# Optimization experiments

Measured on AMD Instinct MI355X. Metric: run time of the kernel, lower is better.

## Reference

```python
import jax, jax.numpy as jnp
import numpy as np

B, M, E, K = 2048, 768, 16384, 32
EPS = 1e-8  # torch F.cosine_similarity default eps


def setup_inputs() -> dict:
    key = jax.random.key(0)
    ks = jax.random.split(key, 13)
    s_m = 1.0 / np.sqrt(M)  # nn.Linear(M, E) init bound
    s_e = 1.0 / np.sqrt(E)  # nn.Linear(E, M) init bound
    u = lambda k, shape, s: jax.random.uniform(k, shape, jnp.float32, -s, s)
    return {
        "x": jax.random.normal(ks[0], (B, M), jnp.float32),
        "enc_w": u(ks[1], (E, M), s_m), "enc_b": u(ks[2], (E,), s_m),
        "dec_w": u(ks[3], (M, E), s_e), "dec_b": u(ks[4], (M,), s_e),
        "enc1_w": u(ks[5], (E, M), s_m), "enc1_b": u(ks[6], (E,), s_m),
        "dec1_w": u(ks[7], (M, E), s_e), "dec1_b": u(ks[8], (M,), s_e),
        "enc2_w": u(ks[9], (E, M), s_m), "enc2_b": u(ks[10], (E,), s_m),
        "dec2_w": u(ks[11], (M, E), s_e), "dec2_b": u(ks[12], (M,), s_e),
        "k": K,
    }


def _aux_loss(a_BE, win_BE, c1_BE, c2_BE, dp_ME, d1_ME, d2_ME):
    # Faithful reduction of the B x M x E cosine-similarity along M:
    #   scaled_parent[b,:,e] = dp[:,e]*a[b,e];  scaled_child uses d1/d2 per winner mask.
    # cos_sim needs only M-dim dot products / norms of decoder columns.
    np2_E = jnp.sum(dp_ME * dp_ME, axis=0)   # ||dp_e||^2
    n1_E = jnp.sum(d1_ME * d1_ME, axis=0)
    n2_E = jnp.sum(d2_ME * d2_ME, axis=0)
    dp1_E = jnp.sum(dp_ME * d1_ME, axis=0)   # <dp_e, d1_e>
    dp2_E = jnp.sum(dp_ME * d2_ME, axis=0)
    c_BE = jnp.where(win_BE, c1_BE, c2_BE)
    dpc_BE = jnp.where(win_BE, dp1_E, dp2_E)
    nc_BE = jnp.where(win_BE, n1_E, n2_E)
    a2 = a_BE * a_BE
    dot = a2 * np2_E + a_BE * c_BE * dpc_BE                      # <parent, parent+child>
    norm_p = jnp.abs(a_BE) * jnp.sqrt(np2_E)                     # ||parent||
    comb2 = a2 * np2_E + 2.0 * a_BE * c_BE * dpc_BE + c_BE * c_BE * nc_BE
    norm_c = jnp.sqrt(jnp.maximum(comb2, 0.0))                   # ||parent+child||
    cos = dot / (jnp.maximum(norm_p, EPS) * jnp.maximum(norm_c, EPS))
    active = a_BE > 0
    return -jnp.sum(jnp.where(active, cos, 0.0)) / a_BE.shape[0]


def reference(x, enc_w, enc_b, dec_w, dec_b, enc1_w, enc1_b, dec1_w, dec1_b,
              enc2_w, enc2_b, dec2_w, dec2_b, k):
    Bn = x.shape[0]
    En = enc_w.shape[0]
    pre_BE = x @ enc_w.T + enc_b
    vals, idx = jax.lax.top_k(pre_BE, k)                         # [B,k]
    sae_BE = jnp.zeros_like(pre_BE).at[jnp.arange(Bn)[:, None], idx].set(vals)
    num_live_parent = jnp.zeros((En,), bool).at[idx.ravel()].set(True).sum()

    pre1_BE = x @ enc1_w.T + enc1_b
    pre2_BE = x @ enc2_w.T + enc2_b
    active = sae_BE != 0.0
    m1_BE = jnp.where(active, pre1_BE, 0.0)
    m2_BE = jnp.where(active, pre2_BE, 0.0)
    win_BE = m1_BE > m2_BE
    f1_BE = jnp.where(win_BE, m1_BE, 0.0)
    f2_BE = jnp.where(~win_BE, m2_BE, 0.0)
    num_live_c1 = jnp.any(f1_BE != 0, axis=0).sum()
    num_live_c2 = jnp.any(f2_BE != 0, axis=0).sum()

    recon_BM = (sae_BE @ dec_w.T + dec_b) + (f1_BE @ dec1_w.T + dec1_b) + (f2_BE @ dec2_w.T + dec2_b)

    sg = jax.lax.stop_gradient
    aux = _aux_loss(sg(sae_BE), sg(win_BE), sg(f1_BE), sg(f2_BE), dec_w, dec1_w, dec2_w)
    return recon_BM, (num_live_parent, num_live_c1, num_live_c2), aux
```

## Files before the change

kernel.cpp:

```cpp
#include <hip/hip_runtime.h>
#include <cstdint>
#include <cstddef>

#define B_N 2048
#define M_N 768
#define E_N 16384
#define K_N 32
#define EPSF 1e-8f

typedef __attribute__((ext_vector_type(8))) short short8;
typedef __attribute__((ext_vector_type(4))) float floatx4;
typedef __attribute__((ext_vector_type(4))) unsigned short ushort4v;

__device__ inline unsigned short f2bf(float f) {
  unsigned int u = __float_as_uint(f);
  unsigned int r = (u + 0x7fffu + ((u >> 16) & 1u)) >> 16;
  return (unsigned short)r;
}
__device__ inline float bf2f(unsigned short h) {
  return __uint_as_float(((unsigned int)h) << 16);
}

__global__ __launch_bounds__(256) void split2_kernel(
    const float* __restrict__ inA, unsigned short* __restrict__ hiA,
    unsigned short* __restrict__ loA, int n4A,
    const float* __restrict__ inB, unsigned short* __restrict__ hiB,
    unsigned short* __restrict__ loB, int n4B) {
  int i = blockIdx.x * 256 + threadIdx.x;
  const float* in;
  unsigned short* hi;
  unsigned short* lo;
  int idx;
  if (i < n4A) {
    in = inA; hi = hiA; lo = loA; idx = i;
  } else {
    idx = i - n4A;
    if (idx >= n4B) return;
    in = inB; hi = hiB; lo = loB;
  }
  float4 v = ((const float4*)in)[idx];
  ushort4v h, l;
  h.x = f2bf(v.x); l.x = f2bf(v.x - bf2f(h.x));
  h.y = f2bf(v.y); l.y = f2bf(v.y - bf2f(h.y));
  h.z = f2bf(v.z); l.z = f2bf(v.z - bf2f(h.z));
  h.w = f2bf(v.w); l.w = f2bf(v.w - bf2f(h.w));
  ((ushort4v*)hi)[idx] = h;
  ((ushort4v*)lo)[idx] = l;
}

__global__ __launch_bounds__(256) void prep_dec_kernel(
    const float* __restrict__ dw, const float* __restrict__ d1,
    const float* __restrict__ d2,
    float* __restrict__ dT0, float* __restrict__ dT1,
    float* __restrict__ dT2, float* __restrict__ stats) {
  __shared__ float t0[32][36], t1[32][36], t2[32][36];
  int tid = threadIdx.x;
  int e0 = blockIdx.x * 32;
  int m0 = blockIdx.y * 32;

  {
    int ml = tid >> 3, e4 = tid & 7;
    size_t gbase = (size_t)(m0 + ml) * E_N + e0 + e4 * 4;
    float4 a  = *(const float4*)&dw[gbase];
    float4 b1 = *(const float4*)&d1[gbase];
    float4 b2 = *(const float4*)&d2[gbase];
    *(float4*)&t0[ml][e4 * 4] = a;
    *(float4*)&t1[ml][e4 * 4] = b1;
    *(float4*)&t2[ml][e4 * 4] = b2;
  }
  __syncthreads();

  int el = tid >> 3, m4 = tid & 7;
  float4 v0, v1, v2;
  float s0 = 0.f, s1 = 0.f, s2 = 0.f, s3 = 0.f, s4 = 0.f;
#pragma unroll
  for (int j = 0; j < 4; ++j) {
    float A  = t0[m4 * 4 + j][el];
    float B1 = t1[m4 * 4 + j][el];
    float B2 = t2[m4 * 4 + j][el];
    ((float*)&v0)[j] = A;
    ((float*)&v1)[j] = B1;
    ((float*)&v2)[j] = B2;
    s0 = fmaf(A, A, s0);
    s1 = fmaf(B1, B1, s1);
    s2 = fmaf(B2, B2, s2);
    s3 = fmaf(A, B1, s3);
    s4 = fmaf(A, B2, s4);
  }
  size_t tbase = (size_t)(e0 + el) * M_N + m0 + m4 * 4;
  *(float4*)&dT0[tbase] = v0;
  *(float4*)&dT1[tbase] = v1;
  *(float4*)&dT2[tbase] = v2;

#pragma unroll
  for (int off = 1; off < 8; off <<= 1) {
    s0 += __shfl_xor(s0, off);
    s1 += __shfl_xor(s1, off);
    s2 += __shfl_xor(s2, off);
    s3 += __shfl_xor(s3, off);
    s4 += __shfl_xor(s4, off);
  }
  if (m4 == 0) {
    int e = e0 + el;
    atomicAdd(&stats[e], s0);
    atomicAdd(&stats[E_N + e], s1);
    atomicAdd(&stats[2 * E_N + e], s2);
    atomicAdd(&stats[3 * E_N + e], s3);
    atomicAdd(&stats[4 * E_N + e], s4);
  }
}

#define TM 128
#define TN 128
#define TK 32
#define LDK 40

__global__ __launch_bounds__(256) void gemm_mfma_kernel(
    const unsigned short* __restrict__ Ahi, const unsigned short* __restrict__ Alo,
    const unsigned short* __restrict__ Bhi, const unsigned short* __restrict__ Blo,
    const float* __restrict__ bias, float* __restrict__ C) {
  __shared__ __align__(16) unsigned short As_hi[TM * LDK];
  __shared__ __align__(16) unsigned short As_lo[TM * LDK];
  __shared__ __align__(16) unsigned short Bs_hi[TM * LDK];
  __shared__ __align__(16) unsigned short Bs_lo[TM * LDK];

  int tid = threadIdx.x;
  int lane = tid & 63;
  int wave = tid >> 6;
  int i0 = blockIdx.y * TM;
  int j0 = blockIdx.x * TN;
  int wm = (wave >> 1) * 64;
  int wn = (wave & 1) * 64;

  int row0 = tid >> 2, c40 = tid & 3;
  int row1 = 64 + (tid >> 2), c41 = tid & 3;
  const unsigned short* pAhi0 = Ahi + (size_t)(i0 + row0) * M_N + c40 * 8;
  const unsigned short* pAhi1 = Ahi + (size_t)(i0 + row1) * M_N + c41 * 8;
  const unsigned short* pAlo0 = Alo + (size_t)(i0 + row0) * M_N + c40 * 8;
  const unsigned short* pAlo1 = Alo + (size_t)(i0 + row1) * M_N + c41 * 8;
  const unsigned short* pBhi0 = Bhi + (size_t)(j0 + row0) * M_N + c40 * 8;
  const unsigned short* pBhi1 = Bhi + (size_t)(j0 + row1) * M_N + c41 * 8;
  const unsigned short* pBlo0 = Blo + (size_t)(j0 + row0) * M_N + c40 * 8;
  const unsigned short* pBlo1 = Blo + (size_t)(j0 + row1) * M_N + c41 * 8;
  int l0 = row0 * LDK + c40 * 8;
  int l1 = row1 * LDK + c41 * 8;

  floatx4 acc[4][4];
#pragma unroll
  for (int i = 0; i < 4; ++i)
#pragma unroll
    for (int j = 0; j < 4; ++j) acc[i][j] = (floatx4){0.f, 0.f, 0.f, 0.f};

  int fr = lane & 15;
  int fk = (lane >> 4) * 8;

  short8 vAh0 = *(const short8*)pAhi0;
  short8 vAh1 = *(const short8*)pAhi1;
  short8 vAl0 = *(const short8*)pAlo0;
  short8 vAl1 = *(const short8*)pAlo1;
  short8 vBh0 = *(const short8*)pBhi0;
  short8 vBh1 = *(const short8*)pBhi1;
  short8 vBl0 = *(const short8*)pBlo0;
  short8 vBl1 = *(const short8*)pBlo1;

  for (int k0 = 0; k0 < M_N; k0 += TK) {
    __syncthreads();
    *(short8*)&As_hi[l0] = vAh0;
    *(short8*)&As_hi[l1] = vAh1;
    *(short8*)&As_lo[l0] = vAl0;
    *(short8*)&As_lo[l1] = vAl1;
    *(short8*)&Bs_hi[l0] = vBh0;
    *(short8*)&Bs_hi[l1] = vBh1;
    *(short8*)&Bs_lo[l0] = vBl0;
    *(short8*)&Bs_lo[l1] = vBl1;
    __syncthreads();

    if (k0 + TK < M_N) {
      int d = k0 + TK;
      vAh0 = *(const short8*)(pAhi0 + d);
      vAh1 = *(const short8*)(pAhi1 + d);
      vAl0 = *(const short8*)(pAlo0 + d);
      vAl1 = *(const short8*)(pAlo1 + d);
      vBh0 = *(const short8*)(pBhi0 + d);
      vBh1 = *(const short8*)(pBhi1 + d);
      vBl0 = *(const short8*)(pBlo0 + d);
      vBl1 = *(const short8*)(pBlo1 + d);
    }

    short8 ah[4], al[4], bh[4], bl[4];
#pragma unroll
    for (int t = 0; t < 4; ++t) {
      int ar = (wm + t * 16 + fr) * LDK + fk;
      int br = (wn + t * 16 + fr) * LDK + fk;
      ah[t] = *(const short8*)&As_hi[ar];
      al[t] = *(const short8*)&As_lo[ar];
      bh[t] = *(const short8*)&Bs_hi[br];
      bl[t] = *(const short8*)&Bs_lo[br];
    }
#pragma unroll
    for (int mi = 0; mi < 4; ++mi)
#pragma unroll
      for (int ni = 0; ni < 4; ++ni) {
        acc[mi][ni] = __builtin_amdgcn_mfma_f32_16x16x32_bf16(ah[mi], bh[ni], acc[mi][ni], 0, 0, 0);
        acc[mi][ni] = __builtin_amdgcn_mfma_f32_16x16x32_bf16(ah[mi], bl[ni], acc[mi][ni], 0, 0, 0);
        acc[mi][ni] = __builtin_amdgcn_mfma_f32_16x16x32_bf16(al[mi], bh[ni], acc[mi][ni], 0, 0, 0);
      }
  }

#pragma unroll
  for (int mi = 0; mi < 4; ++mi) {
    int rbase = i0 + wm + mi * 16 + (lane >> 4) * 4;
#pragma unroll
    for (int ni = 0; ni < 4; ++ni) {
      int col = j0 + wn + ni * 16 + (lane & 15);
      float bb = bias[col];
#pragma unroll
      for (int r = 0; r < 4; ++r) {
        C[(size_t)(rbase + r) * E_N + col] = acc[mi][ni][r] + bb;
      }
    }
  }
}

__global__ __launch_bounds__(256) void topk_kernel(const float* __restrict__ pre,
                                                   int* __restrict__ topk_idx,
                                                   float* __restrict__ topk_val,
                                                   int* __restrict__ live_p) {
  int b = blockIdx.x;
  int tid = threadIdx.x;
  int wave = tid >> 6;
  const float* row = pre + (size_t)b * E_N;

  __shared__ __align__(16) unsigned int hist4[4][2048];
  __shared__ unsigned int csum[256];
  __shared__ float candV[2048];
  __shared__ int candI[2048];
  __shared__ float defV[K_N];
  __shared__ int defI[K_N];
  __shared__ int s_T, s_nDef, s_nCand;

  uint4 z4 = make_uint4(0u, 0u, 0u, 0u);
  uint4* hz = (uint4*)&hist4[0][0];
  for (int i = tid; i < 2048; i += 256) hz[i] = z4;
  if (tid == 0) { s_nDef = 0; s_nCand = 0; }
  __syncthreads();

  for (int j = 0; j < E_N / 1024; ++j) {
    float4 v = ((const float4*)row)[tid + j * 256];
    float f[4] = {v.x, v.y, v.z, v.w};
#pragma unroll
    for (int q = 0; q < 4; ++q) {
      unsigned int u = __float_as_uint(f[q]);
      unsigned int key = (u & 0x80000000u) ? ~u : (u | 0x80000000u);
      atomicAdd(&hist4[wave][key >> 21], 1u);
    }
  }
  __syncthreads();

  unsigned int hm[8];
#pragma unroll
  for (int i = 0; i < 8; ++i) hm[i] = 0u;
#pragma unroll
  for (int w = 0; w < 4; ++w) {
    uint4 p0 = *(const uint4*)&hist4[w][tid * 8];
    uint4 p1 = *(const uint4*)&hist4[w][tid * 8 + 4];
    hm[0] += p0.x; hm[1] += p0.y; hm[2] += p0.z; hm[3] += p0.w;
    hm[4] += p1.x; hm[5] += p1.y; hm[6] += p1.z; hm[7] += p1.w;
  }
  unsigned int sc = hm[0] + hm[1] + hm[2] + hm[3] + hm[4] + hm[5] + hm[6] + hm[7];
  csum[tid] = sc;
  __syncthreads();
  for (int off = 1; off < 256; off <<= 1) {
    unsigned int v_ = (tid + off < 256) ? csum[tid + off] : 0u;
    __syncthreads();
    csum[tid] += v_;
    __syncthreads();
  }
  {
    unsigned int above = (tid < 255) ? csum[tid + 1] : 0u;
    if (csum[tid] >= K_N && above < K_N) {
      unsigned int run = above;
      int T = 0;
#pragma unroll
      for (int i = 7; i >= 0; --i) {
        run += hm[i];
        if (run >= K_N) { T = tid * 8 + i; break; }
      }
      s_T = T;
    }
  }
  __syncthreads();
  int T = s_T;

  for (int j = 0; j < E_N / 1024; ++j) {
    int i4 = tid + j * 256;
    float4 v = ((const float4*)row)[i4];
    float f[4] = {v.x, v.y, v.z, v.w};
#pragma unroll
    for (int q = 0; q < 4; ++q) {
      float vv = f[q];
      unsigned int u = __float_as_uint(vv);
      unsigned int key = (u & 0x80000000u) ? ~u : (u | 0x80000000u);
      int bk = key >> 21;
      if (bk > T) {
        int d = atomicAdd(&s_nDef, 1);
        defV[d] = vv;
        defI[d] = i4 * 4 + q;
      } else if (bk == T) {
        int c = atomicAdd(&s_nCand, 1);
        candV[c] = vv;
        candI[c] = i4 * 4 + q;
      }
    }
  }
  __syncthreads();
  int nDef = s_nDef;
  int nCand = s_nCand;
  int need = K_N - nDef;

  if (tid < nDef) {
    topk_idx[b * K_N + tid] = defI[tid];
    topk_val[b * K_N + tid] = defV[tid];
    live_p[defI[tid]] = 1;
  }
  for (int c = tid; c < nCand; c += 256) {
    float v = candV[c];
    int idx = candI[c];
    int r = 0;
    for (int j2 = 0; j2 < nCand; ++j2) {
      float vj = candV[j2];
      r += (vj > v) || (vj == v && candI[j2] < idx);
    }
    if (r < need) {
      int slot = nDef + r;
      topk_idx[b * K_N + slot] = idx;
      topk_val[b * K_N + slot] = v;
      live_p[idx] = 1;
    }
  }
}

__global__ __launch_bounds__(256, 8) void child_recon_kernel(
    const float* __restrict__ x, const float* __restrict__ e1w, const float* __restrict__ e1b,
    const float* __restrict__ e2w, const float* __restrict__ e2b,
    const int* __restrict__ topk_idx, const float* __restrict__ topk_val,
    int* __restrict__ live_c1, int* __restrict__ live_c2,
    const float* __restrict__ stats, float* __restrict__ aux_sum,
    const float* __restrict__ decT0, const float* __restrict__ decT1,
    const float* __restrict__ decT2,
    const float* __restrict__ db0, const float* __restrict__ db1,
    const float* __restrict__ db2, float* __restrict__ out) {
  int b = blockIdx.x;
  int tid = threadIdx.x;
  int lane = tid & 63;
  int wave = tid >> 6;

  __shared__ float xs[M_N];
  __shared__ int es[K_N];
  __shared__ float as[K_N], cs[K_N];
  __shared__ int wf[K_N];
  __shared__ float wsum[4];

  if (tid < K_N) {
    es[tid] = topk_idx[b * K_N + tid];
    as[tid] = topk_val[b * K_N + tid];
  }
  if (tid < M_N / 4) ((float4*)xs)[tid] = ((const float4*)(x + (size_t)b * M_N))[tid];
  __syncthreads();

  float cos_acc = 0.f;
#pragma unroll
  for (int it = 0; it < 4; ++it) {
    int sA = it * 8 + wave * 2;
    int sB = sA + 1;
    int eA = es[sA], eB = es[sB];
    float aA = as[sA], aB = as[sB];
    const float* w1A = e1w + (size_t)eA * M_N;
    const float* w2A = e2w + (size_t)eA * M_N;
    const float* w1B = e1w + (size_t)eB * M_N;
    const float* w2B = e2w + (size_t)eB * M_N;
    float d1A = 0.f, d2A = 0.f, d1B = 0.f, d2B = 0.f;
#pragma unroll
    for (int j = 0; j < 3; ++j) {
      int m = (lane << 2) + j * 256;
      float4 xv = *(const float4*)&xs[m];
      float4 a1 = *(const float4*)&w1A[m];
      float4 a2 = *(const float4*)&w2A[m];
      float4 b1 = *(const float4*)&w1B[m];
      float4 b2 = *(const float4*)&w2B[m];
      d1A += xv.x * a1.x + xv.y * a1.y + xv.z * a1.z + xv.w * a1.w;
      d2A += xv.x * a2.x + xv.y * a2.y + xv.z * a2.z + xv.w * a2.w;
      d1B += xv.x * b1.x + xv.y * b1.y + xv.z * b1.z + xv.w * b1.w;
      d2B += xv.x * b2.x + xv.y * b2.y + xv.z * b2.z + xv.w * b2.w;
    }
#pragma unroll
    for (int off = 32; off > 0; off >>= 1) {
      d1A += __shfl_down(d1A, off);
      d2A += __shfl_down(d2A, off);
      d1B += __shfl_down(d1B, off);
      d2B += __shfl_down(d2B, off);
    }
    if (lane == 0) {
#pragma unroll
      for (int h = 0; h < 2; ++h) {
        int s = h ? sB : sA;
        int e = h ? eB : eA;
        float a = h ? aB : aA;
        float d1 = h ? d1B : d1A;
        float d2 = h ? d2B : d2A;
        if (a != 0.f) {
          float m1 = d1 + e1b[e];
          float m2 = d2 + e2b[e];
          bool win = m1 > m2;
          float f1 = win ? m1 : 0.f;
          float f2 = win ? 0.f : m2;
          float c = win ? f1 : f2;
          cs[s] = c;
          wf[s] = win ? 1 : 0;
          if (f1 != 0.f) live_c1[e] = 1;
          if (f2 != 0.f) live_c2[e] = 1;
          if (a > 0.f) {
            float np2e = stats[e];
            float nce = win ? stats[E_N + e] : stats[2 * E_N + e];
            float dpc = win ? stats[3 * E_N + e] : stats[4 * E_N + e];
            float a2 = a * a;
            float dot = a2 * np2e + a * c * dpc;
            float normp = fabsf(a) * sqrtf(np2e);
            float comb2 = a2 * np2e + 2.f * a * c * dpc + c * c * nce;
            float normc = sqrtf(fmaxf(comb2, 0.f));
            cos_acc += dot / (fmaxf(normp, EPSF) * fmaxf(normc, EPSF));
          }
        } else {
          cs[s] = 0.f;
          wf[s] = 0;
        }
      }
    }
  }
  if (lane == 0) wsum[wave] = cos_acc;
  __syncthreads();
  if (tid == 0) atomicAdd(aux_sum, wsum[0] + wsum[1] + wsum[2] + wsum[3]);

  float acc0 = db0[tid] + db1[tid] + db2[tid];
  float acc1 = db0[tid + 256] + db1[tid + 256] + db2[tid + 256];
  float acc2 = db0[tid + 512] + db1[tid + 512] + db2[tid + 512];

#pragma unroll 2
  for (int s = 0; s < K_N; ++s) {
    int e = es[s];
    float a = as[s];
    float c = cs[s];
    const float* p = decT0 + (size_t)e * M_N;
    const float* q = (wf[s] ? decT1 : decT2) + (size_t)e * M_N;
    float p0 = p[tid], p1 = p[tid + 256], p2 = p[tid + 512];
    float q0 = q[tid], q1 = q[tid + 256], q2 = q[tid + 512];
    acc0 = fmaf(a, p0, fmaf(c, q0, acc0));
    acc1 = fmaf(a, p1, fmaf(c, q1, acc1));
    acc2 = fmaf(a, p2, fmaf(c, q2, acc2));
  }
  out[(size_t)b * M_N + tid] = acc0;
  out[(size_t)b * M_N + tid + 256] = acc1;
  out[(size_t)b * M_N + tid + 512] = acc2;
}

__global__ void finalize_kernel(const int* __restrict__ live_p, const int* __restrict__ live_c1,
                                const int* __restrict__ live_c2, const float* __restrict__ aux_sum,
                                float* __restrict__ out_tail) {
  int tid = threadIdx.x;
  int c0 = 0, c1 = 0, c2 = 0;
  for (int i = tid; i < E_N; i += 256) {
    c0 += live_p[i];
    c1 += live_c1[i];
    c2 += live_c2[i];
  }
  __shared__ int r0[256], r1[256], r2[256];
  r0[tid] = c0; r1[tid] = c1; r2[tid] = c2;
  __syncthreads();
  for (int s = 128; s > 0; s >>= 1) {
    if (tid < s) { r0[tid] += r0[tid + s]; r1[tid] += r1[tid + s]; r2[tid] += r2[tid + s]; }
    __syncthreads();
  }
  if (tid == 0) {
    out_tail[0] = (float)r0[0];
    out_tail[1] = (float)r1[0];
    out_tail[2] = (float)r2[0];
    out_tail[3] = -aux_sum[0] / (float)B_N;
  }
}

extern "C" void kernel_launch(void* const* d_in, const int* in_sizes, int n_in,
                              void* d_out, int out_size, void* d_ws, size_t ws_size,
                              hipStream_t stream) {
  const float* x     = (const float*)d_in[0];
  const float* enc_w = (const float*)d_in[1];
  const float* enc_b = (const float*)d_in[2];
  const float* dec_w = (const float*)d_in[3];
  const float* dec_b = (const float*)d_in[4];
  const float* e1w   = (const float*)d_in[5];
  const float* e1b   = (const float*)d_in[6];
  const float* d1w   = (const float*)d_in[7];
  const float* d1b   = (const float*)d_in[8];
  const float* e2w   = (const float*)d_in[9];
  const float* e2b   = (const float*)d_in[10];
  const float* d2w   = (const float*)d_in[11];
  const float* d2b   = (const float*)d_in[12];

  float* wsf = (float*)d_ws;

  const size_t PRE_F = (size_t)B_N * E_N;
  const size_t XSP_F = (size_t)B_N * M_N / 2;
  const size_t ESP_F = (size_t)E_N * M_N / 2;
  const size_t DEC_F = (size_t)E_N * M_N;
  const size_t BIG_F = PRE_F + 2 * XSP_F + 2 * ESP_F;

  float* pre = wsf;
  unsigned short* xhi  = (unsigned short*)(wsf + PRE_F);
  unsigned short* xlo  = (unsigned short*)(wsf + PRE_F + XSP_F);
  unsigned short* ewhi = (unsigned short*)(wsf + PRE_F + 2 * XSP_F);
  unsigned short* ewlo = (unsigned short*)(wsf + PRE_F + 2 * XSP_F + ESP_F);
  float* decT0 = wsf;
  float* decT1 = wsf + DEC_F;
  float* decT2 = wsf + 2 * DEC_F;

  size_t off = BIG_F;
  float* stats  = wsf + off;
  int*   livep  = (int*)(wsf + off + 5 * (size_t)E_N);
  int*   livec1 = livep + E_N;
  int*   livec2 = livep + 2 * E_N;
  float* auxs   = (float*)(livep + 3 * E_N);
  off += 8 * (size_t)E_N + 64;
  off &= ~(size_t)63;
  int*   tidx = (int*)(wsf + off);    off += (size_t)B_N * K_N;
  float* tval = wsf + off;            off += (size_t)B_N * K_N;

  hipMemsetAsync(stats, 0, (8 * (size_t)E_N + 1) * sizeof(float), stream);

  int n4A = B_N * M_N / 4;
  int n4B = E_N * M_N / 4;
  split2_kernel<<<(n4A + n4B + 255) / 256, 256, 0, stream>>>(x, xhi, xlo, n4A,
                                                             enc_w, ewhi, ewlo, n4B);

  const int HB = B_N / 2;
  gemm_mfma_kernel<<<dim3(E_N / TN, HB / TM), 256, 0, stream>>>(xhi, xlo, ewhi, ewlo, enc_b, pre);
  gemm_mfma_kernel<<<dim3(E_N / TN, HB / TM), 256, 0, stream>>>(
      xhi + (size_t)HB * M_N, xlo + (size_t)HB * M_N, ewhi, ewlo, enc_b,
      pre + (size_t)HB * E_N);

  topk_kernel<<<B_N, 256, 0, stream>>>(pre, tidx, tval, livep);

  prep_dec_kernel<<<dim3(E_N / 32, M_N / 32), 256, 0, stream>>>(
      dec_w, d1w, d2w, decT0, decT1, decT2, stats);

  float* out = (float*)d_out;
  child_recon_kernel<<<B_N, 256, 0, stream>>>(x, e1w, e1b, e2w, e2b, tidx, tval,
                                              livec1, livec2, stats, auxs,
                                              decT0, decT1, decT2, dec_b, d1b, d2b, out);

  finalize_kernel<<<1, 256, 0, stream>>>(livep, livec1, livec2, auxs,
                                         out + (size_t)B_N * M_N);
}
```

Baseline: 646.4 us.

## Fuse bf16 hi/lo split into GEMM loads and restructure aux cosine reduction

```diff
diff --git a/kernel.cpp b/kernel.cpp
--- a/kernel.cpp
+++ b/kernel.cpp
@@ -10,7 +10,6 @@
 
 typedef __attribute__((ext_vector_type(8))) short short8;
 typedef __attribute__((ext_vector_type(4))) float floatx4;
-typedef __attribute__((ext_vector_type(4))) unsigned short ushort4v;
 
 __device__ inline unsigned short f2bf(float f) {
   unsigned int u = __float_as_uint(f);
@@ -21,31 +20,16 @@
   return __uint_as_float(((unsigned int)h) << 16);
 }
 
-__global__ __launch_bounds__(256) void split2_kernel(
-    const float* __restrict__ inA, unsigned short* __restrict__ hiA,
-    unsigned short* __restrict__ loA, int n4A,
-    const float* __restrict__ inB, unsigned short* __restrict__ hiB,
-    unsigned short* __restrict__ loB, int n4B) {
-  int i = blockIdx.x * 256 + threadIdx.x;
-  const float* in;
-  unsigned short* hi;
-  unsigned short* lo;
-  int idx;
-  if (i < n4A) {
-    in = inA; hi = hiA; lo = loA; idx = i;
-  } else {
-    idx = i - n4A;
-    if (idx >= n4B) return;
-    in = inB; hi = hiB; lo = loB;
-  }
-  float4 v = ((const float4*)in)[idx];
-  ushort4v h, l;
-  h.x = f2bf(v.x); l.x = f2bf(v.x - bf2f(h.x));
-  h.y = f2bf(v.y); l.y = f2bf(v.y - bf2f(h.y));
-  h.z = f2bf(v.z); l.z = f2bf(v.z - bf2f(h.z));
-  h.w = f2bf(v.w); l.w = f2bf(v.w - bf2f(h.w));
-  ((ushort4v*)hi)[idx] = h;
-  ((ushort4v*)lo)[idx] = l;
+__device__ inline void cvt8(const float* __restrict__ p, short8& h8, short8& l8) {
+  float4 v0 = *(const float4*)p;
+  float4 v1 = *(const float4*)(p + 4);
+  float f[8] = {v0.x, v0.y, v0.z, v0.w, v1.x, v1.y, v1.z, v1.w};
+#pragma unroll
+  for (int j = 0; j < 8; ++j) {
+    unsigned short h = f2bf(f[j]);
+    ((unsigned short*)&h8)[j] = h;
+    ((unsigned short*)&l8)[j] = f2bf(f[j] - bf2f(h));
+  }
 }
 
 __global__ __launch_bounds__(256) void prep_dec_kernel(
@@ -116,8 +100,7 @@
 #define LDK 40
 
 __global__ __launch_bounds__(256) void gemm_mfma_kernel(
-    const unsigned short* __restrict__ Ahi, const unsigned short* __restrict__ Alo,
-    const unsigned short* __restrict__ Bhi, const unsigned short* __restrict__ Blo,
+    const float* __restrict__ A, const float* __restrict__ Bm,
     const float* __restrict__ bias, float* __restrict__ C) {
   __shared__ __align__(16) unsigned short As_hi[TM * LDK];
   __shared__ __align__(16) unsigned short As_lo[TM * LDK];
@@ -134,14 +117,10 @@
 
   int row0 = tid >> 2, c40 = tid & 3;
   int row1 = 64 + (tid >> 2), c41 = tid & 3;
-  const unsigned short* pAhi0 = Ahi + (size_t)(i0 + row0) * M_N + c40 * 8;
-  const unsigned short* pAhi1 = Ahi + (size_t)(i0 + row1) * M_N + c41 * 8;
-  const unsigned short* pAlo0 = Alo + (size_t)(i0 + row0) * M_N + c40 * 8;
-  const unsigned short* pAlo1 = Alo + (size_t)(i0 + row1) * M_N + c41 * 8;
-  const unsigned short* pBhi0 = Bhi + (size_t)(j0 + row0) * M_N + c40 * 8;
-  const unsigned short* pBhi1 = Bhi + (size_t)(j0 + row1) * M_N + c41 * 8;
-  const unsigned short* pBlo0 = Blo + (size_t)(j0 + row0) * M_N + c40 * 8;
-  const unsigned short* pBlo1 = Blo + (size_t)(j0 + row1) * M_N + c41 * 8;
+  const float* pA0 = A + (size_t)(i0 + row0) * M_N + c40 * 8;
+  const float* pA1 = A + (size_t)(i0 + row1) * M_N + c41 * 8;
+  const float* pB0 = Bm + (size_t)(j0 + row0) * M_N + c40 * 8;
+  const float* pB1 = Bm + (size_t)(j0 + row1) * M_N + c41 * 8;
   int l0 = row0 * LDK + c40 * 8;
   int l1 = row1 * LDK + c41 * 8;
 
@@ -154,14 +133,11 @@
   int fr = lane & 15;
   int fk = (lane >> 4) * 8;
 
-  short8 vAh0 = *(const short8*)pAhi0;
-  short8 vAh1 = *(const short8*)pAhi1;
-  short8 vAl0 = *(const short8*)pAlo0;
-  short8 vAl1 = *(const short8*)pAlo1;
-  short8 vBh0 = *(const short8*)pBhi0;
-  short8 vBh1 = *(const short8*)pBhi1;
-  short8 vBl0 = *(const short8*)pBlo0;
-  short8 vBl1 = *(const short8*)pBlo1;
+  short8 vAh0, vAl0, vAh1, vAl1, vBh0, vBl0, vBh1, vBl1;
+  cvt8(pA0, vAh0, vAl0);
+  cvt8(pA1, vAh1, vAl1);
+  cvt8(pB0, vBh0, vBl0);
+  cvt8(pB1, vBh1, vBl1);
 
   for (int k0 = 0; k0 < M_N; k0 += TK) {
     __syncthreads();
@@ -177,14 +153,10 @@
 
     if (k0 + TK < M_N) {
       int d = k0 + TK;
-      vAh0 = *(const short8*)(pAhi0 + d);
-      vAh1 = *(const short8*)(pAhi1 + d);
-      vAl0 = *(const short8*)(pAlo0 + d);
-      vAl1 = *(const short8*)(pAlo1 + d);
-      vBh0 = *(const short8*)(pBhi0 + d);
-      vBh1 = *(const short8*)(pBhi1 + d);
-      vBl0 = *(const short8*)(pBlo0 + d);
-      vBl1 = *(const short8*)(pBlo1 + d);
+      cvt8(pA0 + d, vAh0, vAl0);
+      cvt8(pA1 + d, vAh1, vAl1);
+      cvt8(pB0 + d, vBh0, vBl0);
+      cvt8(pB1 + d, vBh1, vBl1);
     }
 
     short8 ah[4], al[4], bh[4], bl[4];
@@ -340,7 +312,7 @@
   }
 }
 
-__global__ __launch_bounds__(256, 8) void child_recon_kernel(
+__global__ __launch_bounds__(256, 6) void child_recon_kernel(
     const float* __restrict__ x, const float* __restrict__ e1w, const float* __restrict__ e1b,
     const float* __restrict__ e2w, const float* __restrict__ e2b,
     const int* __restrict__ topk_idx, const float* __restrict__ topk_val,
@@ -359,7 +331,6 @@
   __shared__ int es[K_N];
   __shared__ float as[K_N], cs[K_N];
   __shared__ int wf[K_N];
-  __shared__ float wsum[4];
 
   if (tid < K_N) {
     es[tid] = topk_idx[b * K_N + tid];
@@ -368,7 +339,6 @@
   if (tid < M_N / 4) ((float4*)xs)[tid] = ((const float4*)(x + (size_t)b * M_N))[tid];
   __syncthreads();
 
-  float cos_acc = 0.f;
 #pragma unroll
   for (int it = 0; it < 4; ++it) {
     int sA = it * 8 + wave * 2;
@@ -419,17 +389,6 @@
           wf[s] = win ? 1 : 0;
           if (f1 != 0.f) live_c1[e] = 1;
           if (f2 != 0.f) live_c2[e] = 1;
-          if (a > 0.f) {
-            float np2e = stats[e];
-            float nce = win ? stats[E_N + e] : stats[2 * E_N + e];
-            float dpc = win ? stats[3 * E_N + e] : stats[4 * E_N + e];
-            float a2 = a * a;
-            float dot = a2 * np2e + a * c * dpc;
-            float normp = fabsf(a) * sqrtf(np2e);
-            float comb2 = a2 * np2e + 2.f * a * c * dpc + c * c * nce;
-            float normc = sqrtf(fmaxf(comb2, 0.f));
-            cos_acc += dot / (fmaxf(normp, EPSF) * fmaxf(normc, EPSF));
-          }
         } else {
           cs[s] = 0.f;
           wf[s] = 0;
@@ -437,15 +396,37 @@
       }
     }
   }
-  if (lane == 0) wsum[wave] = cos_acc;
-  __syncthreads();
-  if (tid == 0) atomicAdd(aux_sum, wsum[0] + wsum[1] + wsum[2] + wsum[3]);
+  __syncthreads();
+
+  float cosv = 0.f;
+  if (tid < K_N) {
+    float a = as[tid];
+    if (a > 0.f) {
+      int e = es[tid];
+      float c = cs[tid];
+      int win = wf[tid];
+      float np2e = stats[e];
+      float nce = win ? stats[E_N + e] : stats[2 * E_N + e];
+      float dpc = win ? stats[3 * E_N + e] : stats[4 * E_N + e];
+      float a2 = a * a;
+      float dot = a2 * np2e + a * c * dpc;
+      float normp = fabsf(a) * sqrtf(np2e);
+      float comb2 = a2 * np2e + 2.f * a * c * dpc + c * c * nce;
+      float normc = sqrtf(fmaxf(comb2, 0.f));
+      cosv = dot / (fmaxf(normp, EPSF) * fmaxf(normc, EPSF));
+    }
+  }
+  if (tid < 64) {
+#pragma unroll
+    for (int off = 32; off > 0; off >>= 1) cosv += __shfl_down(cosv, off);
+    if (tid == 0) atomicAdd(aux_sum, cosv);
+  }
 
   float acc0 = db0[tid] + db1[tid] + db2[tid];
   float acc1 = db0[tid + 256] + db1[tid + 256] + db2[tid + 256];
   float acc2 = db0[tid + 512] + db1[tid + 512] + db2[tid + 512];
 
-#pragma unroll 2
+#pragma unroll 4
   for (int s = 0; s < K_N; ++s) {
     int e = es[s];
     float a = as[s];
@@ -508,16 +489,10 @@
   float* wsf = (float*)d_ws;
 
   const size_t PRE_F = (size_t)B_N * E_N;
-  const size_t XSP_F = (size_t)B_N * M_N / 2;
-  const size_t ESP_F = (size_t)E_N * M_N / 2;
   const size_t DEC_F = (size_t)E_N * M_N;
-  const size_t BIG_F = PRE_F + 2 * XSP_F + 2 * ESP_F;
+  const size_t BIG_F = (PRE_F > 3 * DEC_F) ? PRE_F : 3 * DEC_F;
 
   float* pre = wsf;
-  unsigned short* xhi  = (unsigned short*)(wsf + PRE_F);
-  unsigned short* xlo  = (unsigned short*)(wsf + PRE_F + XSP_F);
-  unsigned short* ewhi = (unsigned short*)(wsf + PRE_F + 2 * XSP_F);
-  unsigned short* ewlo = (unsigned short*)(wsf + PRE_F + 2 * XSP_F + ESP_F);
   float* decT0 = wsf;
   float* decT1 = wsf + DEC_F;
   float* decT2 = wsf + 2 * DEC_F;
@@ -535,16 +510,10 @@
 
   hipMemsetAsync(stats, 0, (8 * (size_t)E_N + 1) * sizeof(float), stream);
 
-  int n4A = B_N * M_N / 4;
-  int n4B = E_N * M_N / 4;
-  split2_kernel<<<(n4A + n4B + 255) / 256, 256, 0, stream>>>(x, xhi, xlo, n4A,
-                                                             enc_w, ewhi, ewlo, n4B);
-
   const int HB = B_N / 2;
-  gemm_mfma_kernel<<<dim3(E_N / TN, HB / TM), 256, 0, stream>>>(xhi, xlo, ewhi, ewlo, enc_b, pre);
+  gemm_mfma_kernel<<<dim3(E_N / TN, HB / TM), 256, 0, stream>>>(x, enc_w, enc_b, pre);
   gemm_mfma_kernel<<<dim3(E_N / TN, HB / TM), 256, 0, stream>>>(
-      xhi + (size_t)HB * M_N, xlo + (size_t)HB * M_N, ewhi, ewlo, enc_b,
-      pre + (size_t)HB * E_N);
+      x + (size_t)HB * M_N, enc_w, enc_b, pre + (size_t)HB * E_N);
 
   topk_kernel<<<B_N, 256, 0, stream>>>(pre, tidx, tval, livep);
 
```

Result: slower. 676.5 us (+4.6%).
